# Optimization experiments

Measured on AMD Instinct MI355X. Metric: run time of the kernel, lower is better.

## Reference

```python
import jax, jax.numpy as jnp
import numpy as np

N_POS = 8192
BATCH = 4
N_GT = 512
EPS = 1e-6
P_EXP = -1.0  # generalized-mean exponent (p < 0)


def setup_inputs() -> dict:
    key = jax.random.key(0)
    k1, k2, k3 = jax.random.split(key, 3)
    dis_matrix = jax.random.uniform(k1, (N_POS, N_POS), dtype=jnp.float32)
    prob_map = jax.random.uniform(k2, (BATCH, N_POS), dtype=jnp.float32)
    gt = jax.random.randint(k3, (BATCH, N_GT), 0, N_POS, dtype=jnp.int64 if jax.config.jax_enable_x64 else jnp.int32)
    return {"prob_map": prob_map, "gt": gt, "dis_matrix": dis_matrix}


def reference(prob_map, gt, dis_matrix):
    max_dist = jnp.max(dis_matrix)
    # global min-max normalization with detached min/range (matches torch .detach())
    pmin = jax.lax.stop_gradient(jnp.min(prob_map))
    prange = jax.lax.stop_gradient(jnp.max(prob_map) - jnp.min(prob_map))
    prob = jnp.clip((prob_map - pmin) / prange, 0.0, 1.0)  # (B, N)

    # gather gt-indexed columns: dis_matrix[:, gt] -> (N, B, G) -> (B, N, G)
    D = jnp.transpose(jnp.take(dis_matrix, gt, axis=1), (1, 0, 2))

    n_est = prob.sum(axis=1)  # (B,)
    # term 1: (1/n_est) * sum_n p_n * min_g D[n, g]
    term1 = jnp.sum(prob * jnp.min(D, axis=2), axis=1) / (n_est + EPS)  # (B,)

    # term 2: generalized mean over pixel dim of weighted distance matrix
    w = (1.0 - prob)[:, :, None] * max_dist + prob[:, :, None] * D  # (B, N, G)
    minn = jnp.mean((w + EPS) ** P_EXP, axis=1) ** (1.0 / P_EXP)  # (B, G)
    term2 = jnp.mean(minn, axis=1)  # (B,)

    return jnp.mean(term1) + jnp.mean(term2)
```

## Files before the change

kernel.cpp:

```cpp
#include <hip/hip_runtime.h>
#include <math.h>

#define N_POS 8192
#define BATCH 4
#define N_GT 512
#define BG 2048
#define EPSV 1e-6f

#define KA_BLOCKS 1024
#define ROWS_A 8
#define KC_BLOCKS 1024
#define ROWS_C 8
#define RG 32
#define CHUNKS_PER_RG (KC_BLOCKS / RG)

#define WS_DPACK 0
#define WS_PARTS (N_POS * BG)
#define WS_PARTS2 (WS_PARTS + KC_BLOCKS * BG)
#define WS_MIND  (WS_PARTS2 + RG * BG)
#define WS_MAXP  (WS_MIND + 8 * N_POS)
#define WS_SC    (WS_MAXP + KA_BLOCKS)

typedef __attribute__((ext_vector_type(4))) float f32x4;

__device__ __forceinline__ void rowbar() {
    asm volatile("s_waitcnt lgkmcnt(0)" ::: "memory");
    __builtin_amdgcn_s_barrier();
    asm volatile("" ::: "memory");
}

__global__ __launch_bounds__(512) void whd_kA(const float* __restrict__ dis,
                                              const int* __restrict__ gt,
                                              float* __restrict__ wsf) {
    __shared__ float rowbuf[2][N_POS];
    __shared__ float smax[8];
    const int t = threadIdx.x;
    const int wv = t >> 6, lane = t & 63;
    const int row0 = blockIdx.x * ROWS_A;
    float* dpack = wsf + WS_DPACK;
    float* minD2 = wsf + WS_MIND;

    int c[4];
    {
        const int4 ci = ((const int4*)gt)[t];
        c[0] = ci.x; c[1] = ci.y; c[2] = ci.z; c[3] = ci.w;
    }

    f32x4 preA[4], preB[4];
    {
        const f32x4* s0 = (const f32x4*)(dis + (size_t)row0 * N_POS);
        const f32x4* s1 = (const f32x4*)(dis + (size_t)(row0 + 1) * N_POS);
        #pragma unroll
        for (int j = 0; j < 4; j++) preA[j] = __builtin_nontemporal_load(s0 + t + 512 * j);
        #pragma unroll
        for (int j = 0; j < 4; j++) preB[j] = __builtin_nontemporal_load(s1 + t + 512 * j);
    }

    float tmax = -INFINITY;
    #pragma unroll
    for (int r = 0; r < ROWS_A; r++) {
        const int n = row0 + r;
        float* buf = rowbuf[r & 1];
        if ((r & 1) == 0) {
            #pragma unroll
            for (int j = 0; j < 4; j++) ((f32x4*)buf)[t + 512 * j] = preA[j];
            #pragma unroll
            for (int j = 0; j < 4; j++)
                tmax = fmaxf(tmax, fmaxf(fmaxf(preA[j].x, preA[j].y), fmaxf(preA[j].z, preA[j].w)));
            if (r + 2 < ROWS_A) {
                const f32x4* sn = (const f32x4*)(dis + (size_t)(n + 2) * N_POS);
                #pragma unroll
                for (int j = 0; j < 4; j++) preA[j] = __builtin_nontemporal_load(sn + t + 512 * j);
            }
        } else {
            #pragma unroll
            for (int j = 0; j < 4; j++) ((f32x4*)buf)[t + 512 * j] = preB[j];
            #pragma unroll
            for (int j = 0; j < 4; j++)
                tmax = fmaxf(tmax, fmaxf(fmaxf(preB[j].x, preB[j].y), fmaxf(preB[j].z, preB[j].w)));
            if (r + 2 < ROWS_A) {
                const f32x4* sn = (const f32x4*)(dis + (size_t)(n + 2) * N_POS);
                #pragma unroll
                for (int j = 0; j < 4; j++) preB[j] = __builtin_nontemporal_load(sn + t + 512 * j);
            }
        }
        rowbar();
        float g0 = buf[c[0]], g1 = buf[c[1]], g2 = buf[c[2]], g3 = buf[c[3]];
        f32x4 pk; pk.x = g0; pk.y = g1; pk.z = g2; pk.w = g3;
        ((f32x4*)(dpack + (size_t)n * BG + 4 * t))[0] = pk;
        float m = fminf(fminf(g0, g1), fminf(g2, g3));
        #pragma unroll
        for (int off = 32; off; off >>= 1) m = fminf(m, __shfl_xor(m, off, 64));
        if (lane == 0) minD2[(size_t)wv * N_POS + n] = m;
    }
    #pragma unroll
    for (int off = 32; off; off >>= 1) tmax = fmaxf(tmax, __shfl_down(tmax, off, 64));
    if (lane == 0) smax[wv] = tmax;
    __syncthreads();
    if (t == 0) {
        float m = smax[0];
        #pragma unroll
        for (int i = 1; i < 8; i++) m = fmaxf(m, smax[i]);
        wsf[WS_MAXP + blockIdx.x] = m;
    }
}

__global__ __launch_bounds__(1024) void whd_kB(const float* __restrict__ prob,
                                               float* __restrict__ wsf) {
    __shared__ float sA[16], sB[16], sC[16];
    const int t = threadIdx.x, wv = t >> 6, lane = t & 63;

    float m = -INFINITY;
    for (int i = t; i < KA_BLOCKS; i += 1024) m = fmaxf(m, wsf[WS_MAXP + i]);
    #pragma unroll
    for (int off = 32; off; off >>= 1) m = fmaxf(m, __shfl_xor(m, off, 64));

    float lmin = INFINITY, lmax = -INFINITY;
    const f32x4* p4 = (const f32x4*)prob;
    for (int i = t; i < BATCH * N_POS / 4; i += 1024) {
        f32x4 v = p4[i];
        lmin = fminf(fminf(lmin, fminf(v.x, v.y)), fminf(v.z, v.w));
        lmax = fmaxf(fmaxf(lmax, fmaxf(v.x, v.y)), fmaxf(v.z, v.w));
    }
    #pragma unroll
    for (int off = 32; off; off >>= 1) {
        lmin = fminf(lmin, __shfl_xor(lmin, off, 64));
        lmax = fmaxf(lmax, __shfl_xor(lmax, off, 64));
    }
    if (lane == 0) { sA[wv] = m; sB[wv] = lmin; sC[wv] = lmax; }
    __syncthreads();
    if (t == 0) {
        float maxd = -INFINITY, mn = INFINITY, mx = -INFINITY;
        #pragma unroll
        for (int i = 0; i < 16; i++) {
            maxd = fmaxf(maxd, sA[i]); mn = fminf(mn, sB[i]); mx = fmaxf(mx, sC[i]);
        }
        wsf[WS_SC + 0] = maxd;
        wsf[WS_SC + 1] = mn;
        wsf[WS_SC + 2] = mx - mn;
        wsf[WS_SC + 11] = 0.f;
        wsf[WS_SC + 12] = 0.f;
        sB[0] = mn; sC[0] = 1.0f / (mx - mn);
    }
    __syncthreads();
    const float pmin = sB[0], invr = sC[0];

    for (int b = 0; b < BATCH; b++) {
        const f32x4* dA = (const f32x4*)(wsf + WS_MIND + (size_t)(2 * b) * N_POS);
        const f32x4* dB = (const f32x4*)(wsf + WS_MIND + (size_t)(2 * b + 1) * N_POS);
        float sp = 0.f, spm = 0.f;
        for (int i = t; i < N_POS / 4; i += 1024) {
            f32x4 v = p4[b * (N_POS / 4) + i];
            f32x4 da = dA[i], db = dB[i];
            float p;
            p = fminf(fmaxf((v.x - pmin) * invr, 0.f), 1.f); sp += p; spm += p * fminf(da.x, db.x);
            p = fminf(fmaxf((v.y - pmin) * invr, 0.f), 1.f); sp += p; spm += p * fminf(da.y, db.y);
            p = fminf(fmaxf((v.z - pmin) * invr, 0.f), 1.f); sp += p; spm += p * fminf(da.z, db.z);
            p = fminf(fmaxf((v.w - pmin) * invr, 0.f), 1.f); sp += p; spm += p * fminf(da.w, db.w);
        }
        #pragma unroll
        for (int off = 32; off; off >>= 1) {
            sp += __shfl_xor(sp, off, 64);
            spm += __shfl_xor(spm, off, 64);
        }
        __syncthreads();
        if (lane == 0) { sA[wv] = sp; sB[wv] = spm; }
        __syncthreads();
        if (t == 0) {
            float a = 0.f, c2 = 0.f;
            #pragma unroll
            for (int i = 0; i < 16; i++) { a += sA[i]; c2 += sB[i]; }
            wsf[WS_SC + 3 + b] = a;
            wsf[WS_SC + 7 + b] = c2;
        }
    }
}

__global__ __launch_bounds__(256) void whd_kC(const float* __restrict__ prob,
                                              float* __restrict__ wsf) {
    const int t = threadIdx.x;
    const int wv = t >> 6;
    const int row0 = blockIdx.x * ROWS_C;
    const float* dpack = wsf + WS_DPACK;
    const float maxd = wsf[WS_SC + 0];
    const float pmin = wsf[WS_SC + 1];
    const float invr = 1.0f / wsf[WS_SC + 2];
    float acc[8];
    #pragma unroll
    for (int k = 0; k < 8; k++) acc[k] = 0.f;
    #pragma unroll
    for (int r = 0; r < ROWS_C; r++) {
        const int n = row0 + r;
        float p = (prob[wv * N_POS + n] - pmin) * invr;
        p = fminf(fmaxf(p, 0.f), 1.f);
        const f32x4* rp = (const f32x4*)(dpack + (size_t)n * BG + 8 * t);
        f32x4 v0 = __builtin_nontemporal_load(rp);
        f32x4 v1 = __builtin_nontemporal_load(rp + 1);
        acc[0] += 1.0f / (fmaf(p, v0.x - maxd, maxd) + EPSV);
        acc[1] += 1.0f / (fmaf(p, v0.y - maxd, maxd) + EPSV);
        acc[2] += 1.0f / (fmaf(p, v0.z - maxd, maxd) + EPSV);
        acc[3] += 1.0f / (fmaf(p, v0.w - maxd, maxd) + EPSV);
        acc[4] += 1.0f / (fmaf(p, v1.x - maxd, maxd) + EPSV);
        acc[5] += 1.0f / (fmaf(p, v1.y - maxd, maxd) + EPSV);
        acc[6] += 1.0f / (fmaf(p, v1.z - maxd, maxd) + EPSV);
        acc[7] += 1.0f / (fmaf(p, v1.w - maxd, maxd) + EPSV);
    }
    f32x4* op = (f32x4*)(wsf + WS_PARTS + (size_t)blockIdx.x * BG + 8 * t);
    f32x4 o0; o0.x = acc[0]; o0.y = acc[1]; o0.z = acc[2]; o0.w = acc[3];
    f32x4 o1; o1.x = acc[4]; o1.y = acc[5]; o1.z = acc[6]; o1.w = acc[7];
    op[0] = o0;
    op[1] = o1;
}

__global__ __launch_bounds__(256) void whd_kD1(float* __restrict__ wsf) {
    const int t = threadIdx.x;
    const int col = blockIdx.x * 256 + t;
    const int rg = blockIdx.y;
    const float* parts = wsf + WS_PARTS + (size_t)rg * CHUNKS_PER_RG * BG;
    float s = 0.f;
    #pragma unroll 8
    for (int ch = 0; ch < CHUNKS_PER_RG; ch++) s += parts[(size_t)ch * BG + col];
    wsf[WS_PARTS2 + (size_t)rg * BG + col] = s;
}

__global__ __launch_bounds__(256) void whd_kD2(float* __restrict__ wsf,
                                               float* __restrict__ out) {
    __shared__ float red[4];
    const int t = threadIdx.x;
    const int col = blockIdx.x * 256 + t;
    const float* p2 = wsf + WS_PARTS2;
    float s = 0.f;
    #pragma unroll
    for (int rg = 0; rg < RG; rg++) s += p2[(size_t)rg * BG + col];
    float val = (float)N_POS / s;
    #pragma unroll
    for (int off = 32; off; off >>= 1) val += __shfl_xor(val, off, 64);
    if ((t & 63) == 0) red[t >> 6] = val;
    __syncthreads();
    if (t == 0) {
        float blocksum = red[0] + red[1] + red[2] + red[3];
        atomicAdd(&wsf[WS_SC + 11], blocksum);
        __threadfence();
        unsigned prev = atomicAdd((unsigned*)(wsf + WS_SC + 12), 1u);
        if (prev == gridDim.x - 1) {
            float t2sum = atomicAdd(&wsf[WS_SC + 11], 0.0f);
            float term1 = 0.f;
            #pragma unroll
            for (int b = 0; b < BATCH; b++)
                term1 += wsf[WS_SC + 7 + b] / (wsf[WS_SC + 3 + b] + EPSV);
            out[0] = term1 * (1.0f / BATCH) + t2sum * (1.0f / BG);
        }
    }
}

extern "C" void kernel_launch(void* const* d_in, const int* in_sizes, int n_in,
                              void* d_out, int out_size, void* d_ws, size_t ws_size,
                              hipStream_t stream) {
    const float* prob = (const float*)d_in[0];
    const int* gt = (const int*)d_in[1];
    const float* dis = (const float*)d_in[2];
    float* out = (float*)d_out;
    float* wsf = (float*)d_ws;

    whd_kA<<<KA_BLOCKS, 512, 0, stream>>>(dis, gt, wsf);
    whd_kB<<<1, 1024, 0, stream>>>(prob, wsf);
    whd_kC<<<KC_BLOCKS, 256, 0, stream>>>(prob, wsf);
    whd_kD1<<<dim3(BG / 256, RG), 256, 0, stream>>>(wsf);
    whd_kD2<<<BG / 256, 256, 0, stream>>>(wsf, out);
}
```

Measured before the change: 397.7 us.

## Deepen row prefetch in kA, enlarge kC row chunks and drop kD1 reduction

Kernel A now keeps four rows of the distance matrix in flight instead of two, using a 4-slot register ring to hide more HBM latency. Kernel C processes 32 rows per block across 256 blocks, cutting the partial-sum buffer fourfold, and its packed loads become normal cached loads. The intermediate kD1 reduction launch is removed, so kD2 sums 256 partials per column directly. This trades register pressure in kA, and a longer serial reduction on only 8 blocks in kD2, for less launch overhead and less partial traffic.

```diff
diff --git a/kernel.cpp b/kernel.cpp
--- a/kernel.cpp
+++ b/kernel.cpp
@@ -9,15 +9,12 @@
 
 #define KA_BLOCKS 1024
 #define ROWS_A 8
-#define KC_BLOCKS 1024
-#define ROWS_C 8
-#define RG 32
-#define CHUNKS_PER_RG (KC_BLOCKS / RG)
+#define KC_BLOCKS 256
+#define ROWS_C 32
 
 #define WS_DPACK 0
 #define WS_PARTS (N_POS * BG)
-#define WS_PARTS2 (WS_PARTS + KC_BLOCKS * BG)
-#define WS_MIND  (WS_PARTS2 + RG * BG)
+#define WS_MIND  (WS_PARTS + KC_BLOCKS * BG)
 #define WS_MAXP  (WS_MIND + 8 * N_POS)
 #define WS_SC    (WS_MAXP + KA_BLOCKS)
 
@@ -46,43 +43,30 @@
         c[0] = ci.x; c[1] = ci.y; c[2] = ci.z; c[3] = ci.w;
     }
 
-    f32x4 preA[4], preB[4];
-    {
-        const f32x4* s0 = (const f32x4*)(dis + (size_t)row0 * N_POS);
-        const f32x4* s1 = (const f32x4*)(dis + (size_t)(row0 + 1) * N_POS);
-        #pragma unroll
-        for (int j = 0; j < 4; j++) preA[j] = __builtin_nontemporal_load(s0 + t + 512 * j);
-        #pragma unroll
-        for (int j = 0; j < 4; j++) preB[j] = __builtin_nontemporal_load(s1 + t + 512 * j);
+    f32x4 pre[4][4];
+    #pragma unroll
+    for (int b = 0; b < 4; b++) {
+        const f32x4* s = (const f32x4*)(dis + (size_t)(row0 + b) * N_POS);
+        #pragma unroll
+        for (int j = 0; j < 4; j++) pre[b][j] = __builtin_nontemporal_load(s + t + 512 * j);
     }
 
     float tmax = -INFINITY;
     #pragma unroll
     for (int r = 0; r < ROWS_A; r++) {
         const int n = row0 + r;
+        const int bk = r & 3;
         float* buf = rowbuf[r & 1];
-        if ((r & 1) == 0) {
+        #pragma unroll
+        for (int j = 0; j < 4; j++) ((f32x4*)buf)[t + 512 * j] = pre[bk][j];
+        #pragma unroll
+        for (int j = 0; j < 4; j++)
+            tmax = fmaxf(tmax, fmaxf(fmaxf(pre[bk][j].x, pre[bk][j].y),
+                                     fmaxf(pre[bk][j].z, pre[bk][j].w)));
+        if (r + 4 < ROWS_A) {
+            const f32x4* sn = (const f32x4*)(dis + (size_t)(n + 4) * N_POS);
             #pragma unroll
-            for (int j = 0; j < 4; j++) ((f32x4*)buf)[t + 512 * j] = preA[j];
-            #pragma unroll
-            for (int j = 0; j < 4; j++)
-                tmax = fmaxf(tmax, fmaxf(fmaxf(preA[j].x, preA[j].y), fmaxf(preA[j].z, preA[j].w)));
-            if (r + 2 < ROWS_A) {
-                const f32x4* sn = (const f32x4*)(dis + (size_t)(n + 2) * N_POS);
-                #pragma unroll
-                for (int j = 0; j < 4; j++) preA[j] = __builtin_nontemporal_load(sn + t + 512 * j);
-            }
-        } else {
-            #pragma unroll
-            for (int j = 0; j < 4; j++) ((f32x4*)buf)[t + 512 * j] = preB[j];
-            #pragma unroll
-            for (int j = 0; j < 4; j++)
-                tmax = fmaxf(tmax, fmaxf(fmaxf(preB[j].x, preB[j].y), fmaxf(preB[j].z, preB[j].w)));
-            if (r + 2 < ROWS_A) {
-                const f32x4* sn = (const f32x4*)(dis + (size_t)(n + 2) * N_POS);
-                #pragma unroll
-                for (int j = 0; j < 4; j++) preB[j] = __builtin_nontemporal_load(sn + t + 512 * j);
-            }
+            for (int j = 0; j < 4; j++) pre[bk][j] = __builtin_nontemporal_load(sn + t + 512 * j);
         }
         rowbar();
         float g0 = buf[c[0]], g1 = buf[c[1]], g2 = buf[c[2]], g3 = buf[c[3]];
@@ -188,14 +172,14 @@
     float acc[8];
     #pragma unroll
     for (int k = 0; k < 8; k++) acc[k] = 0.f;
-    #pragma unroll
+    #pragma unroll 8
     for (int r = 0; r < ROWS_C; r++) {
         const int n = row0 + r;
         float p = (prob[wv * N_POS + n] - pmin) * invr;
         p = fminf(fmaxf(p, 0.f), 1.f);
         const f32x4* rp = (const f32x4*)(dpack + (size_t)n * BG + 8 * t);
-        f32x4 v0 = __builtin_nontemporal_load(rp);
-        f32x4 v1 = __builtin_nontemporal_load(rp + 1);
+        f32x4 v0 = rp[0];
+        f32x4 v1 = rp[1];
         acc[0] += 1.0f / (fmaf(p, v0.x - maxd, maxd) + EPSV);
         acc[1] += 1.0f / (fmaf(p, v0.y - maxd, maxd) + EPSV);
         acc[2] += 1.0f / (fmaf(p, v0.z - maxd, maxd) + EPSV);
@@ -212,26 +196,15 @@
     op[1] = o1;
 }
 
-__global__ __launch_bounds__(256) void whd_kD1(float* __restrict__ wsf) {
-    const int t = threadIdx.x;
-    const int col = blockIdx.x * 256 + t;
-    const int rg = blockIdx.y;
-    const float* parts = wsf + WS_PARTS + (size_t)rg * CHUNKS_PER_RG * BG;
-    float s = 0.f;
-    #pragma unroll 8
-    for (int ch = 0; ch < CHUNKS_PER_RG; ch++) s += parts[(size_t)ch * BG + col];
-    wsf[WS_PARTS2 + (size_t)rg * BG + col] = s;
-}
-
 __global__ __launch_bounds__(256) void whd_kD2(float* __restrict__ wsf,
                                                float* __restrict__ out) {
     __shared__ float red[4];
     const int t = threadIdx.x;
     const int col = blockIdx.x * 256 + t;
-    const float* p2 = wsf + WS_PARTS2;
+    const float* parts = wsf + WS_PARTS;
     float s = 0.f;
-    #pragma unroll
-    for (int rg = 0; rg < RG; rg++) s += p2[(size_t)rg * BG + col];
+    #pragma unroll 8
+    for (int ch = 0; ch < KC_BLOCKS; ch++) s += parts[(size_t)ch * BG + col];
     float val = (float)N_POS / s;
     #pragma unroll
     for (int off = 32; off; off >>= 1) val += __shfl_xor(val, off, 64);
@@ -265,6 +238,5 @@
     whd_kA<<<KA_BLOCKS, 512, 0, stream>>>(dis, gt, wsf);
     whd_kB<<<1, 1024, 0, stream>>>(prob, wsf);
     whd_kC<<<KC_BLOCKS, 256, 0, stream>>>(prob, wsf);
-    whd_kD1<<<dim3(BG / 256, RG), 256, 0, stream>>>(wsf);
     whd_kD2<<<BG / 256, 256, 0, stream>>>(wsf, out);
 }
```

After: 408.8 us. 2.8% more time.
